# Kernel optimization log

Measured on AMD Instinct MI355X. Metric: run time of the kernel, lower is better.

Reference implementation:

```python
import jax, jax.numpy as jnp
import numpy as np
from math import sqrt

B, L, S, H, E, D = 2, 2048, 2048, 16, 64, 64

def setup_inputs() -> dict:
    key = jax.random.key(0)
    kq, kk, kv = jax.random.split(key, 3)
    queries = jax.random.normal(kq, (B, L, H, E), dtype=jnp.float32)
    keys = jax.random.normal(kk, (B, S, H, E), dtype=jnp.float32)
    values = jax.random.normal(kv, (B, S, H, D), dtype=jnp.float32)
    # causal mask: True where attention is NOT allowed (j > i), matching masked_fill_ semantics
    causal = jnp.triu(jnp.ones((L, S), dtype=jnp.bool_), k=1)
    attn_mask = jnp.broadcast_to(causal[None, None, :, :], (B, 1, L, S))
    return {"queries": queries, "keys": keys, "values": values, "attn_mask": attn_mask}

def reference(queries, keys, values, attn_mask):
    # scores: [B,H,L,S]
    scale = 1.0 / sqrt(queries.shape[-1])
    scores = jnp.einsum('blhe,bshe->bhls', queries, keys)
    scores = jnp.where(attn_mask, -jnp.inf, scores)
    A = jax.nn.softmax(scale * scores, axis=-1)
    V = jnp.einsum('bhls,bshd->blhd', A, values)
    return V
```

## Files before the change

kernel.cpp:

```cpp
#include <hip/hip_runtime.h>

typedef unsigned short ushort_t;
typedef __attribute__((ext_vector_type(8))) short s8v;
typedef __attribute__((ext_vector_type(2))) unsigned u2v;
typedef __attribute__((ext_vector_type(4))) float f4;

__device__ __forceinline__ ushort_t f2bf(float x) {
    unsigned u = __builtin_bit_cast(unsigned, x);
    return (ushort_t)((u + 0x7FFFu + ((u >> 16) & 1u)) >> 16);
}
__device__ __forceinline__ unsigned pack_hi16(float lo, float hi) {
    unsigned a = __builtin_bit_cast(unsigned, lo);
    unsigned b = __builtin_bit_cast(unsigned, hi);
    return (a >> 16) | (b & 0xFFFF0000u);
}

__global__ __launch_bounds__(256) void prep_kv(const float* __restrict__ K,
                                               const float* __restrict__ V,
                                               ushort_t* __restrict__ Kb,
                                               ushort_t* __restrict__ VT) {
    __shared__ ushort_t T[64 * 72];
    if (blockIdx.x < 2048) {
        const int gid = blockIdx.x * 256 + threadIdx.x;
        const int e = (gid & 7) * 8;
        const int h = (gid >> 3) & 15;
        const int s = (gid >> 7) & 2047;
        const int b = gid >> 18;
        const float* src = K + (((b * 2048 + s) * 16 + h) * 64 + e);
        f4 a = *(const f4*)src;
        f4 c = *(const f4*)(src + 4);
        s8v o;
        #pragma unroll
        for (int j = 0; j < 4; ++j) { o[j] = (short)f2bf(a[j]); o[j + 4] = (short)f2bf(c[j]); }
        *(s8v*)(Kb + (((b * 16 + h) * 2048 + s) * 64 + e)) = o;
    } else {
        const int v = blockIdx.x - 2048;
        const int s0 = (v & 31) * 64;
        const int h  = (v >> 5) & 15;
        const int b  = v >> 9;
        const int t  = threadIdx.x;
        {
            const int srow = t >> 2, dc = (t & 3) * 16;
            const float* src = V + (((b * 2048 + s0 + srow) * 16 + h) * 64 + dc);
            #pragma unroll
            for (int c = 0; c < 4; ++c) {
                f4 vv = *(const f4*)(src + c * 4);
                #pragma unroll
                for (int j = 0; j < 4; ++j) T[(dc + c * 4 + j) * 72 + srow] = f2bf(vv[j]);
            }
        }
        __syncthreads();
        {
            const int d = t >> 2, sq = (t & 3) * 16;
            ushort_t* dst = VT + (((b * 16 + h) * 64 + d) * 2048 + s0 + sq);
            *(s8v*)(dst)     = *(const s8v*)(&T[d * 72 + sq]);
            *(s8v*)(dst + 8) = *(const s8v*)(&T[d * 72 + sq + 8]);
        }
    }
}

__global__ __launch_bounds__(128, 2) void fattn_main(
    const float* __restrict__ Q,
    const ushort_t* __restrict__ Kb,
    const ushort_t* __restrict__ VTb,
    float* __restrict__ O)
{
    constexpr float K1 = 0.18033688011112042f;
    constexpr float SHIFT = 12.0f;
    __shared__ ushort_t KT [64 * 72];
    __shared__ ushort_t VTl[64 * 72];
    __shared__ ushort_t P  [4][16 * 72];

    const int bx = blockIdx.x;
    const int bh = bx & 31;
    const int g  = bx >> 5, c8 = g & 7, j4 = g >> 3;
    const int i  = (j4 == 0) ? c8 : (j4 == 1) ? 31 - c8 : (j4 == 2) ? 15 - c8 : 16 + c8;
    const int b = bh >> 4, h = bh & 15;
    const int qr0 = i * 64;
    const int il  = i;

    const int wave = threadIdx.x >> 6;
    const int lane = threadIdx.x & 63;
    const int l15  = lane & 15;
    const int quad = lane >> 4;

    const ushort_t* kb  = Kb  + bh * (2048 * 64);
    const ushort_t* vtb = VTb + bh * (64 * 2048);
    const float*    qb  = Q + b * (2048 * 1024) + h * 64;
    float*          ob  = O + b * (2048 * 1024) + h * 64;

    const s8v ones = {0x3F80, 0x3F80, 0x3F80, 0x3F80, 0x3F80, 0x3F80, 0x3F80, 0x3F80};
    const f4 zero4 = {0.f, 0.f, 0.f, 0.f};

    const int sr = (wave << 5) + (lane >> 1);
    const int sc = (lane & 1) << 5;

    s8v aq[2][2];
    #pragma unroll
    for (int m = 0; m < 2; ++m) {
        const float* qrow = qb + (qr0 + wave * 32 + m * 16 + l15) * 1024;
        #pragma unroll
        for (int ks = 0; ks < 2; ++ks) {
            f4 x = *(const f4*)(qrow + ks * 32 + quad * 8);
            f4 y = *(const f4*)(qrow + ks * 32 + quad * 8 + 4);
            #pragma unroll
            for (int j = 0; j < 4; ++j) {
                aq[m][ks][j]     = (short)f2bf(x[j]);
                aq[m][ks][j + 4] = (short)f2bf(y[j]);
            }
        }
    }

    f4 oacc[2][4];
    f4 lsum[2] = {zero4, zero4};
    #pragma unroll
    for (int m = 0; m < 2; ++m)
        #pragma unroll
        for (int d = 0; d < 4; ++d) oacc[m][d] = zero4;

    s8v gK[4], gV[4];
    {
        const ushort_t* ksrc = kb + sr * 64 + sc;
        const ushort_t* vsrc = vtb + sr * 2048 + sc;
        #pragma unroll
        for (int c = 0; c < 4; ++c) {
            gK[c] = *(const s8v*)(ksrc + c * 8);
            gV[c] = *(const s8v*)(vsrc + c * 8);
        }
    }

    for (int it = 0; it <= il; ++it) {
        #pragma unroll
        for (int c = 0; c < 4; ++c) {
            *(s8v*)&KT [sr * 72 + sc + c * 8] = gK[c];
            *(s8v*)&VTl[sr * 72 + sc + c * 8] = gV[c];
        }
        __syncthreads();

        s8v gK2[4], gV2[4];
        if (it < il) {
            const ushort_t* ksrc = kb + ((it + 1) * 64 + sr) * 64 + sc;
            const ushort_t* vsrc = vtb + sr * 2048 + (it + 1) * 64 + sc;
            #pragma unroll
            for (int c = 0; c < 4; ++c) {
                gK2[c] = *(const s8v*)(ksrc + c * 8);
                gV2[c] = *(const s8v*)(vsrc + c * 8);
            }
        }

        const int n0 = it * 64;
        const bool diag = (it == il);

        f4 st[2][4];
        #pragma unroll
        for (int t = 0; t < 4; ++t) {
            const s8v bk0 = *(const s8v*)&KT[(t * 16 + l15) * 72 + quad * 8];
            const s8v bk1 = *(const s8v*)&KT[(t * 16 + l15) * 72 + 32 + quad * 8];
            #pragma unroll
            for (int m = 0; m < 2; ++m) {
                f4 a = __builtin_amdgcn_mfma_f32_16x16x32_bf16(bk0, aq[m][0], zero4, 0, 0, 0);
                st[m][t] = __builtin_amdgcn_mfma_f32_16x16x32_bf16(bk1, aq[m][1], a, 0, 0, 0);
            }
        }

        #pragma unroll
        for (int m = 0; m < 2; ++m) {
            ushort_t* Pm = P[wave * 2 + m];
            #pragma unroll
            for (int t = 0; t < 4; ++t) {
                float p[4];
                #pragma unroll
                for (int r = 0; r < 4; ++r) {
                    float x = __builtin_fmaf(st[m][t][r], K1, -SHIFT);
                    if (diag) {
                        const int gj = n0 + t * 16 + quad * 4 + r;
                        const int gi = qr0 + wave * 32 + m * 16 + l15;
                        if (gj > gi) x = -INFINITY;
                    }
                    p[r] = __builtin_exp2f(x);
                }
                u2v pk;
                pk[0] = pack_hi16(p[0], p[1]);
                pk[1] = pack_hi16(p[2], p[3]);
                *(u2v*)&Pm[l15 * 72 + t * 16 + quad * 4] = pk;
            }
        }

        #pragma unroll
        for (int ks = 0; ks < 2; ++ks) {
            s8v bvv[4];
            #pragma unroll
            for (int dd = 0; dd < 4; ++dd)
                bvv[dd] = *(const s8v*)&VTl[(dd * 16 + l15) * 72 + ks * 32 + quad * 8];
            #pragma unroll
            for (int m = 0; m < 2; ++m) {
                const s8v ap = *(const s8v*)&P[wave * 2 + m][l15 * 72 + ks * 32 + quad * 8];
                lsum[m] = __builtin_amdgcn_mfma_f32_16x16x32_bf16(ap, ones, lsum[m], 0, 0, 0);
                #pragma unroll
                for (int dd = 0; dd < 4; ++dd)
                    oacc[m][dd] = __builtin_amdgcn_mfma_f32_16x16x32_bf16(ap, bvv[dd], oacc[m][dd], 0, 0, 0);
            }
        }

        __syncthreads();

        if (it < il) {
            #pragma unroll
            for (int c = 0; c < 4; ++c) { gK[c] = gK2[c]; gV[c] = gV2[c]; }
        }
    }

    #pragma unroll
    for (int m = 0; m < 2; ++m)
        #pragma unroll
        for (int r = 0; r < 4; ++r) {
            const float inv = 1.0f / lsum[m][r];
            const int row = qr0 + wave * 32 + m * 16 + quad * 4 + r;
            #pragma unroll
            for (int dd = 0; dd < 4; ++dd)
                ob[row * 1024 + dd * 16 + l15] = oacc[m][dd][r] * inv;
        }
}

#define PSTR 72
__global__ __launch_bounds__(256) void fattn_fallback(
    const float* __restrict__ Q, const float* __restrict__ K,
    const float* __restrict__ V, float* __restrict__ O)
{
    constexpr int strL = 1024, strB = 2048 * strL;
    const float scale = 0.125f;
    __shared__ ushort_t KT[64 * PSTR];
    __shared__ ushort_t VT[64 * PSTR];
    __shared__ ushort_t P[4][16 * PSTR];
    const int bh = blockIdx.x & 31;
    const int b = bh >> 4, h = bh & 15;
    const int im = 31 - (blockIdx.x >> 5);
    const int q0 = im * 64;
    const int tid = threadIdx.x, wave = tid >> 6, lane = tid & 63;
    const int l15 = lane & 15, quad = lane >> 4;
    const float* qbase = Q + b*strB + (q0 + wave*16 + l15)*strL + h*64;
    s8v aq0, aq1;
    {
        f4 q0v = *(const f4*)(qbase + quad*8);
        f4 q1v = *(const f4*)(qbase + quad*8 + 4);
        f4 q2v = *(const f4*)(qbase + 32 + quad*8);
        f4 q3v = *(const f4*)(qbase + 32 + quad*8 + 4);
        #pragma unroll
        for (int j = 0; j < 4; ++j) {
            aq0[j] = (short)f2bf(q0v[j]); aq0[j+4] = (short)f2bf(q1v[j]);
            aq1[j] = (short)f2bf(q2v[j]); aq1[j+4] = (short)f2bf(q3v[j]);
        }
    }
    const f4 zero4 = {0.f,0.f,0.f,0.f};
    f4 oacc[4]; float m_prev[4], lsum[4];
    #pragma unroll
    for (int d = 0; d < 4; ++d) oacc[d] = zero4;
    #pragma unroll
    for (int r = 0; r < 4; ++r) { m_prev[r] = -INFINITY; lsum[r] = 0.0f; }
    const float* kh = K + b*strB + h*64;
    const float* vh = V + b*strB + h*64;
    for (int it = 0; it <= im; ++it) {
        const int n0 = it * 64;
        __syncthreads();
        {
            const float* krow = kh + (n0 + lane)*strL + wave*16;
            f4 k0 = *(const f4*)(krow); f4 k1 = *(const f4*)(krow+4);
            f4 k2 = *(const f4*)(krow+8); f4 k3 = *(const f4*)(krow+12);
            s8v kb0, kb1;
            #pragma unroll
            for (int j = 0; j < 4; ++j) {
                kb0[j] = (short)f2bf(k0[j]); kb0[j+4] = (short)f2bf(k1[j]);
                kb1[j] = (short)f2bf(k2[j]); kb1[j+4] = (short)f2bf(k3[j]);
            }
            *(s8v*)&KT[lane*PSTR + wave*16] = kb0;
            *(s8v*)&KT[lane*PSTR + wave*16 + 8] = kb1;
            const float* vrow = vh + (n0 + lane)*strL + wave*16;
            f4 v0 = *(const f4*)(vrow); f4 v1 = *(const f4*)(vrow+4);
            f4 v2 = *(const f4*)(vrow+8); f4 v3 = *(const f4*)(vrow+12);
            #pragma unroll
            for (int j = 0; j < 4; ++j) {
                VT[(wave*16 + j)*PSTR + lane] = f2bf(v0[j]);
                VT[(wave*16 + 4 + j)*PSTR + lane] = f2bf(v1[j]);
                VT[(wave*16 + 8 + j)*PSTR + lane] = f2bf(v2[j]);
                VT[(wave*16 + 12 + j)*PSTR + lane] = f2bf(v3[j]);
            }
        }
        __syncthreads();
        f4 sacc[4];
        #pragma unroll
        for (int t = 0; t < 4; ++t) {
            sacc[t] = zero4;
            const s8v bk0 = *(const s8v*)&KT[(t*16 + l15)*PSTR + quad*8];
            const s8v bk1 = *(const s8v*)&KT[(t*16 + l15)*PSTR + 32 + quad*8];
            sacc[t] = __builtin_amdgcn_mfma_f32_16x16x32_bf16(aq0, bk0, sacc[t], 0, 0, 0);
            sacc[t] = __builtin_amdgcn_mfma_f32_16x16x32_bf16(aq1, bk1, sacc[t], 0, 0, 0);
        }
        const bool diag = (it == im);
        float sv[4][4], rmax[4];
        #pragma unroll
        for (int r = 0; r < 4; ++r) rmax[r] = -INFINITY;
        #pragma unroll
        for (int t = 0; t < 4; ++t)
            #pragma unroll
            for (int r = 0; r < 4; ++r) {
                float x = sacc[t][r] * scale;
                if (diag) {
                    const int gi = wave*16 + quad*4 + r;
                    const int gj = t*16 + l15;
                    if (gj > gi) x = -INFINITY;
                }
                sv[t][r] = x; rmax[r] = fmaxf(rmax[r], x);
            }
        #pragma unroll
        for (int off = 8; off >= 1; off >>= 1)
            #pragma unroll
            for (int r = 0; r < 4; ++r)
                rmax[r] = fmaxf(rmax[r], __shfl_xor(rmax[r], off, 64));
        float mnew[4], alpha[4], rsum[4];
        #pragma unroll
        for (int r = 0; r < 4; ++r) {
            mnew[r] = fmaxf(m_prev[r], rmax[r]);
            alpha[r] = __expf(m_prev[r] - mnew[r]);
            m_prev[r] = mnew[r]; rsum[r] = 0.f;
        }
        #pragma unroll
        for (int t = 0; t < 4; ++t)
            #pragma unroll
            for (int r = 0; r < 4; ++r) {
                const float p = __expf(sv[t][r] - mnew[r]);
                rsum[r] += p;
                P[wave][(quad*4 + r)*PSTR + t*16 + l15] = f2bf(p);
            }
        #pragma unroll
        for (int off = 8; off >= 1; off >>= 1)
            #pragma unroll
            for (int r = 0; r < 4; ++r)
                rsum[r] += __shfl_xor(rsum[r], off, 64);
        #pragma unroll
        for (int r = 0; r < 4; ++r) lsum[r] = alpha[r]*lsum[r] + rsum[r];
        #pragma unroll
        for (int d = 0; d < 4; ++d)
            #pragma unroll
            for (int r = 0; r < 4; ++r) oacc[d][r] *= alpha[r];
        #pragma unroll
        for (int ks = 0; ks < 2; ++ks) {
            const s8v ap = *(const s8v*)&P[wave][l15*PSTR + ks*32 + quad*8];
            #pragma unroll
            for (int d = 0; d < 4; ++d) {
                const s8v bvv = *(const s8v*)&VT[(d*16 + l15)*PSTR + ks*32 + quad*8];
                oacc[d] = __builtin_amdgcn_mfma_f32_16x16x32_bf16(ap, bvv, oacc[d], 0, 0, 0);
            }
        }
    }
    float* obase = O + b*strB + h*64;
    #pragma unroll
    for (int r = 0; r < 4; ++r) {
        const float inv = 1.0f / lsum[r];
        const int gi = q0 + wave*16 + quad*4 + r;
        #pragma unroll
        for (int d = 0; d < 4; ++d)
            obase[gi*strL + d*16 + l15] = oacc[d][r] * inv;
    }
}

extern "C" void kernel_launch(void* const* d_in, const int* in_sizes, int n_in,
                              void* d_out, int out_size, void* d_ws, size_t ws_size,
                              hipStream_t stream) {
    const float* Q = (const float*)d_in[0];
    const float* K = (const float*)d_in[1];
    const float* V = (const float*)d_in[2];
    float* O = (float*)d_out;
    const size_t NEED = 2ull * 4194304ull * 2ull;
    if (ws_size >= NEED) {
        ushort_t* Kb = (ushort_t*)d_ws;
        ushort_t* VT = Kb + 4194304;
        prep_kv<<<3072, 256, 0, stream>>>(K, V, Kb, VT);
        fattn_main<<<1024, 128, 0, stream>>>(Q, Kb, VT, O);
    } else {
        fattn_fallback<<<1024, 256, 0, stream>>>(Q, K, V, O);
    }
}
```

Before: 153.7 us.

## Pair causal query tiles per block with four waves of sixteen rows

Each block now processes two complementary query tiles (p and 31-p) sequentially, so every block runs exactly 33 KV iterations, balancing causal work across blocks. Block size doubles to 256 threads with each wave owning 16 query rows instead of 32, and the grid halves to 512 blocks. This removes load imbalance from the triangular workload and the tail effect, at the cost of fewer blocks, half the MFMA work per K/V tile load per wave, and a store/reload of Q mid-loop.

```diff
diff --git a/kernel.cpp b/kernel.cpp
--- a/kernel.cpp
+++ b/kernel.cpp
@@ -59,7 +59,7 @@
     }
 }
 
-__global__ __launch_bounds__(128, 2) void fattn_main(
+__global__ __launch_bounds__(256, 2) void fattn_main(
     const float* __restrict__ Q,
     const ushort_t* __restrict__ Kb,
     const ushort_t* __restrict__ VTb,
@@ -73,11 +73,8 @@
 
     const int bx = blockIdx.x;
     const int bh = bx & 31;
-    const int g  = bx >> 5, c8 = g & 7, j4 = g >> 3;
-    const int i  = (j4 == 0) ? c8 : (j4 == 1) ? 31 - c8 : (j4 == 2) ? 15 - c8 : 16 + c8;
+    const int p  = bx >> 5;
     const int b = bh >> 4, h = bh & 15;
-    const int qr0 = i * 64;
-    const int il  = i;
 
     const int wave = threadIdx.x >> 6;
     const int lane = threadIdx.x & 63;
@@ -92,98 +89,102 @@
     const s8v ones = {0x3F80, 0x3F80, 0x3F80, 0x3F80, 0x3F80, 0x3F80, 0x3F80, 0x3F80};
     const f4 zero4 = {0.f, 0.f, 0.f, 0.f};
 
-    const int sr = (wave << 5) + (lane >> 1);
-    const int sc = (lane & 1) << 5;
-
-    s8v aq[2][2];
-    #pragma unroll
-    for (int m = 0; m < 2; ++m) {
-        const float* qrow = qb + (qr0 + wave * 32 + m * 16 + l15) * 1024;
+    const int sr = threadIdx.x >> 2;
+    const int sc = (threadIdx.x & 3) << 4;
+
+    int qr0 = p * 64;
+
+    s8v aq[2];
+    f4 oacc[4];
+    f4 lsum;
+
+    auto loadQ = [&](int qr) {
+        const float* qrow = qb + (qr + wave * 16 + l15) * 1024;
         #pragma unroll
         for (int ks = 0; ks < 2; ++ks) {
             f4 x = *(const f4*)(qrow + ks * 32 + quad * 8);
             f4 y = *(const f4*)(qrow + ks * 32 + quad * 8 + 4);
             #pragma unroll
             for (int j = 0; j < 4; ++j) {
-                aq[m][ks][j]     = (short)f2bf(x[j]);
-                aq[m][ks][j + 4] = (short)f2bf(y[j]);
-            }
-        }
-    }
-
-    f4 oacc[2][4];
-    f4 lsum[2] = {zero4, zero4};
-    #pragma unroll
-    for (int m = 0; m < 2; ++m)
-        #pragma unroll
-        for (int d = 0; d < 4; ++d) oacc[m][d] = zero4;
-
-    s8v gK[4], gV[4];
+                aq[ks][j]     = (short)f2bf(x[j]);
+                aq[ks][j + 4] = (short)f2bf(y[j]);
+            }
+        }
+    };
+    auto zeroAcc = [&]() {
+        lsum = zero4;
+        #pragma unroll
+        for (int d = 0; d < 4; ++d) oacc[d] = zero4;
+    };
+    auto storeO = [&](int qr) {
+        #pragma unroll
+        for (int r = 0; r < 4; ++r) {
+            const float inv = 1.0f / lsum[r];
+            const int row = qr + wave * 16 + quad * 4 + r;
+            #pragma unroll
+            for (int dd = 0; dd < 4; ++dd)
+                ob[row * 1024 + dd * 16 + l15] = oacc[dd][r] * inv;
+        }
+    };
+
+    loadQ(qr0);
+    zeroAcc();
+
+    s8v gK[2], gV[2];
     {
         const ushort_t* ksrc = kb + sr * 64 + sc;
         const ushort_t* vsrc = vtb + sr * 2048 + sc;
-        #pragma unroll
-        for (int c = 0; c < 4; ++c) {
-            gK[c] = *(const s8v*)(ksrc + c * 8);
-            gV[c] = *(const s8v*)(vsrc + c * 8);
-        }
-    }
-
-    for (int it = 0; it <= il; ++it) {
-        #pragma unroll
-        for (int c = 0; c < 4; ++c) {
-            *(s8v*)&KT [sr * 72 + sc + c * 8] = gK[c];
-            *(s8v*)&VTl[sr * 72 + sc + c * 8] = gV[c];
-        }
-        __syncthreads();
-
-        s8v gK2[4], gV2[4];
-        if (it < il) {
-            const ushort_t* ksrc = kb + ((it + 1) * 64 + sr) * 64 + sc;
-            const ushort_t* vsrc = vtb + sr * 2048 + (it + 1) * 64 + sc;
-            #pragma unroll
-            for (int c = 0; c < 4; ++c) {
-                gK2[c] = *(const s8v*)(ksrc + c * 8);
-                gV2[c] = *(const s8v*)(vsrc + c * 8);
-            }
-        }
-
-        const int n0 = it * 64;
-        const bool diag = (it == il);
-
-        f4 st[2][4];
+        gK[0] = *(const s8v*)(ksrc);     gK[1] = *(const s8v*)(ksrc + 8);
+        gV[0] = *(const s8v*)(vsrc);     gV[1] = *(const s8v*)(vsrc + 8);
+    }
+
+    for (int n = 0; n < 33; ++n) {
+        *(s8v*)&KT [sr * 72 + sc]     = gK[0];
+        *(s8v*)&KT [sr * 72 + sc + 8] = gK[1];
+        *(s8v*)&VTl[sr * 72 + sc]     = gV[0];
+        *(s8v*)&VTl[sr * 72 + sc + 8] = gV[1];
+        __syncthreads();
+
+        s8v gK2[2], gV2[2];
+        if (n < 32) {
+            const int sn = (n + 1 <= p) ? (n + 1) : (n - p);
+            const ushort_t* ksrc = kb + (sn * 64 + sr) * 64 + sc;
+            const ushort_t* vsrc = vtb + sr * 2048 + sn * 64 + sc;
+            gK2[0] = *(const s8v*)(ksrc);    gK2[1] = *(const s8v*)(ksrc + 8);
+            gV2[0] = *(const s8v*)(vsrc);    gV2[1] = *(const s8v*)(vsrc + 8);
+        }
+
+        const int s_cur = (n <= p) ? n : (n - p - 1);
+        const int n0 = s_cur * 64;
+        const bool diag = (n == p) || (n == 32);
+
+        f4 st[4];
         #pragma unroll
         for (int t = 0; t < 4; ++t) {
             const s8v bk0 = *(const s8v*)&KT[(t * 16 + l15) * 72 + quad * 8];
             const s8v bk1 = *(const s8v*)&KT[(t * 16 + l15) * 72 + 32 + quad * 8];
-            #pragma unroll
-            for (int m = 0; m < 2; ++m) {
-                f4 a = __builtin_amdgcn_mfma_f32_16x16x32_bf16(bk0, aq[m][0], zero4, 0, 0, 0);
-                st[m][t] = __builtin_amdgcn_mfma_f32_16x16x32_bf16(bk1, aq[m][1], a, 0, 0, 0);
-            }
-        }
-
-        #pragma unroll
-        for (int m = 0; m < 2; ++m) {
-            ushort_t* Pm = P[wave * 2 + m];
-            #pragma unroll
-            for (int t = 0; t < 4; ++t) {
-                float p[4];
-                #pragma unroll
-                for (int r = 0; r < 4; ++r) {
-                    float x = __builtin_fmaf(st[m][t][r], K1, -SHIFT);
-                    if (diag) {
-                        const int gj = n0 + t * 16 + quad * 4 + r;
-                        const int gi = qr0 + wave * 32 + m * 16 + l15;
-                        if (gj > gi) x = -INFINITY;
-                    }
-                    p[r] = __builtin_exp2f(x);
+            f4 a = __builtin_amdgcn_mfma_f32_16x16x32_bf16(bk0, aq[0], zero4, 0, 0, 0);
+            st[t] = __builtin_amdgcn_mfma_f32_16x16x32_bf16(bk1, aq[1], a, 0, 0, 0);
+        }
+
+        ushort_t* Pm = P[wave];
+        #pragma unroll
+        for (int t = 0; t < 4; ++t) {
+            float pv[4];
+            #pragma unroll
+            for (int r = 0; r < 4; ++r) {
+                float x = __builtin_fmaf(st[t][r], K1, -SHIFT);
+                if (diag) {
+                    const int gj = n0 + t * 16 + quad * 4 + r;
+                    const int gi = qr0 + wave * 16 + l15;
+                    if (gj > gi) x = -INFINITY;
                 }
-                u2v pk;
-                pk[0] = pack_hi16(p[0], p[1]);
-                pk[1] = pack_hi16(p[2], p[3]);
-                *(u2v*)&Pm[l15 * 72 + t * 16 + quad * 4] = pk;
-            }
+                pv[r] = __builtin_exp2f(x);
+            }
+            u2v pk;
+            pk[0] = pack_hi16(pv[0], pv[1]);
+            pk[1] = pack_hi16(pv[2], pv[3]);
+            *(u2v*)&Pm[l15 * 72 + t * 16 + quad * 4] = pk;
         }
 
         #pragma unroll
@@ -192,34 +193,29 @@
             #pragma unroll
             for (int dd = 0; dd < 4; ++dd)
                 bvv[dd] = *(const s8v*)&VTl[(dd * 16 + l15) * 72 + ks * 32 + quad * 8];
-            #pragma unroll
-            for (int m = 0; m < 2; ++m) {
-                const s8v ap = *(const s8v*)&P[wave * 2 + m][l15 * 72 + ks * 32 + quad * 8];
-                lsum[m] = __builtin_amdgcn_mfma_f32_16x16x32_bf16(ap, ones, lsum[m], 0, 0, 0);
-                #pragma unroll
-                for (int dd = 0; dd < 4; ++dd)
-                    oacc[m][dd] = __builtin_amdgcn_mfma_f32_16x16x32_bf16(ap, bvv[dd], oacc[m][dd], 0, 0, 0);
-            }
-        }
-
-        __syncthreads();
-
-        if (it < il) {
-            #pragma unroll
-            for (int c = 0; c < 4; ++c) { gK[c] = gK2[c]; gV[c] = gV2[c]; }
-        }
-    }
-
-    #pragma unroll
-    for (int m = 0; m < 2; ++m)
-        #pragma unroll
-        for (int r = 0; r < 4; ++r) {
-            const float inv = 1.0f / lsum[m][r];
-            const int row = qr0 + wave * 32 + m * 16 + quad * 4 + r;
+            const s8v ap = *(const s8v*)&Pm[l15 * 72 + ks * 32 + quad * 8];
+            lsum = __builtin_amdgcn_mfma_f32_16x16x32_bf16(ap, ones, lsum, 0, 0, 0);
             #pragma unroll
             for (int dd = 0; dd < 4; ++dd)
-                ob[row * 1024 + dd * 16 + l15] = oacc[m][dd][r] * inv;
-        }
+                oacc[dd] = __builtin_amdgcn_mfma_f32_16x16x32_bf16(ap, bvv[dd], oacc[dd], 0, 0, 0);
+        }
+
+        __syncthreads();
+
+        if (n < 32) {
+            gK[0] = gK2[0]; gK[1] = gK2[1];
+            gV[0] = gV2[0]; gV[1] = gV2[1];
+        }
+
+        if (n == p) {
+            storeO(qr0);
+            qr0 = (31 - p) * 64;
+            loadQ(qr0);
+            zeroAcc();
+        }
+    }
+
+    storeO(qr0);
 }
 
 #define PSTR 72
@@ -375,7 +371,7 @@
         ushort_t* Kb = (ushort_t*)d_ws;
         ushort_t* VT = Kb + 4194304;
         prep_kv<<<3072, 256, 0, stream>>>(K, V, Kb, VT);
-        fattn_main<<<1024, 128, 0, stream>>>(Q, Kb, VT, O);
+        fattn_main<<<512, 256, 0, stream>>>(Q, Kb, VT, O);
     } else {
         fattn_fallback<<<1024, 256, 0, stream>>>(Q, K, V, O);
     }
```

Result: no change. 151.8 us (-1.2%).

## Pair complementary causal query tiles per block for balanced work

Applied to the files above, without the earlier changes.

Each block now handles query tile p and then tile 31-p in one continuous loop of 33 KV iterations, storing the first tile's output and reloading Q in the middle. The grid halves to 512 blocks, so every block does the same amount of work and the causal triangle no longer leaves uneven tail blocks. In exchange there is less parallelism, 512 blocks of 128 threads on a 256-CU device, and a serial dependency where the Q reload sits inside the loop.

```diff
diff --git a/kernel.cpp b/kernel.cpp
--- a/kernel.cpp
+++ b/kernel.cpp
@@ -73,11 +73,8 @@
 
     const int bx = blockIdx.x;
     const int bh = bx & 31;
-    const int g  = bx >> 5, c8 = g & 7, j4 = g >> 3;
-    const int i  = (j4 == 0) ? c8 : (j4 == 1) ? 31 - c8 : (j4 == 2) ? 15 - c8 : 16 + c8;
+    const int p  = bx >> 5;
     const int b = bh >> 4, h = bh & 15;
-    const int qr0 = i * 64;
-    const int il  = i;
 
     const int wave = threadIdx.x >> 6;
     const int lane = threadIdx.x & 63;
@@ -95,28 +92,51 @@
     const int sr = (wave << 5) + (lane >> 1);
     const int sc = (lane & 1) << 5;
 
+    int qr0 = p * 64;
+
     s8v aq[2][2];
-    #pragma unroll
-    for (int m = 0; m < 2; ++m) {
-        const float* qrow = qb + (qr0 + wave * 32 + m * 16 + l15) * 1024;
-        #pragma unroll
-        for (int ks = 0; ks < 2; ++ks) {
-            f4 x = *(const f4*)(qrow + ks * 32 + quad * 8);
-            f4 y = *(const f4*)(qrow + ks * 32 + quad * 8 + 4);
-            #pragma unroll
-            for (int j = 0; j < 4; ++j) {
-                aq[m][ks][j]     = (short)f2bf(x[j]);
-                aq[m][ks][j + 4] = (short)f2bf(y[j]);
-            }
-        }
-    }
-
     f4 oacc[2][4];
-    f4 lsum[2] = {zero4, zero4};
-    #pragma unroll
-    for (int m = 0; m < 2; ++m)
-        #pragma unroll
-        for (int d = 0; d < 4; ++d) oacc[m][d] = zero4;
+    f4 lsum[2];
+
+    auto loadQ = [&](int qr) {
+        #pragma unroll
+        for (int m = 0; m < 2; ++m) {
+            const float* qrow = qb + (qr + wave * 32 + m * 16 + l15) * 1024;
+            #pragma unroll
+            for (int ks = 0; ks < 2; ++ks) {
+                f4 x = *(const f4*)(qrow + ks * 32 + quad * 8);
+                f4 y = *(const f4*)(qrow + ks * 32 + quad * 8 + 4);
+                #pragma unroll
+                for (int j = 0; j < 4; ++j) {
+                    aq[m][ks][j]     = (short)f2bf(x[j]);
+                    aq[m][ks][j + 4] = (short)f2bf(y[j]);
+                }
+            }
+        }
+    };
+    auto zeroAcc = [&]() {
+        #pragma unroll
+        for (int m = 0; m < 2; ++m) {
+            lsum[m] = zero4;
+            #pragma unroll
+            for (int d = 0; d < 4; ++d) oacc[m][d] = zero4;
+        }
+    };
+    auto storeO = [&](int qr) {
+        #pragma unroll
+        for (int m = 0; m < 2; ++m)
+            #pragma unroll
+            for (int r = 0; r < 4; ++r) {
+                const float inv = 1.0f / lsum[m][r];
+                const int row = qr + wave * 32 + m * 16 + quad * 4 + r;
+                #pragma unroll
+                for (int dd = 0; dd < 4; ++dd)
+                    ob[row * 1024 + dd * 16 + l15] = oacc[m][dd][r] * inv;
+            }
+    };
+
+    loadQ(qr0);
+    zeroAcc();
 
     s8v gK[4], gV[4];
     {
@@ -129,7 +149,7 @@
         }
     }
 
-    for (int it = 0; it <= il; ++it) {
+    for (int n = 0; n < 33; ++n) {
         #pragma unroll
         for (int c = 0; c < 4; ++c) {
             *(s8v*)&KT [sr * 72 + sc + c * 8] = gK[c];
@@ -138,9 +158,10 @@
         __syncthreads();
 
         s8v gK2[4], gV2[4];
-        if (it < il) {
-            const ushort_t* ksrc = kb + ((it + 1) * 64 + sr) * 64 + sc;
-            const ushort_t* vsrc = vtb + sr * 2048 + (it + 1) * 64 + sc;
+        if (n < 32) {
+            const int sn = (n + 1 <= p) ? (n + 1) : (n - p);
+            const ushort_t* ksrc = kb + (sn * 64 + sr) * 64 + sc;
+            const ushort_t* vsrc = vtb + sr * 2048 + sn * 64 + sc;
             #pragma unroll
             for (int c = 0; c < 4; ++c) {
                 gK2[c] = *(const s8v*)(ksrc + c * 8);
@@ -148,8 +169,9 @@
             }
         }
 
-        const int n0 = it * 64;
-        const bool diag = (it == il);
+        const int s_cur = (n <= p) ? n : (n - p - 1);
+        const int n0 = s_cur * 64;
+        const bool diag = (n == p) || (n == 32);
 
         f4 st[2][4];
         #pragma unroll
@@ -168,7 +190,7 @@
             ushort_t* Pm = P[wave * 2 + m];
             #pragma unroll
             for (int t = 0; t < 4; ++t) {
-                float p[4];
+                float pv[4];
                 #pragma unroll
                 for (int r = 0; r < 4; ++r) {
                     float x = __builtin_fmaf(st[m][t][r], K1, -SHIFT);
@@ -177,11 +199,11 @@
                         const int gi = qr0 + wave * 32 + m * 16 + l15;
                         if (gj > gi) x = -INFINITY;
                     }
-                    p[r] = __builtin_exp2f(x);
+                    pv[r] = __builtin_exp2f(x);
                 }
                 u2v pk;
-                pk[0] = pack_hi16(p[0], p[1]);
-                pk[1] = pack_hi16(p[2], p[3]);
+                pk[0] = pack_hi16(pv[0], pv[1]);
+                pk[1] = pack_hi16(pv[2], pv[3]);
                 *(u2v*)&Pm[l15 * 72 + t * 16 + quad * 4] = pk;
             }
         }
@@ -204,22 +226,20 @@
 
         __syncthreads();
 
-        if (it < il) {
+        if (n < 32) {
             #pragma unroll
             for (int c = 0; c < 4; ++c) { gK[c] = gK2[c]; gV[c] = gV2[c]; }
         }
-    }
-
-    #pragma unroll
-    for (int m = 0; m < 2; ++m)
-        #pragma unroll
-        for (int r = 0; r < 4; ++r) {
-            const float inv = 1.0f / lsum[m][r];
-            const int row = qr0 + wave * 32 + m * 16 + quad * 4 + r;
-            #pragma unroll
-            for (int dd = 0; dd < 4; ++dd)
-                ob[row * 1024 + dd * 16 + l15] = oacc[m][dd][r] * inv;
-        }
+
+        if (n == p) {
+            storeO(qr0);
+            qr0 = (31 - p) * 64;
+            loadQ(qr0);
+            zeroAcc();
+        }
+    }
+
+    storeO(qr0);
 }
 
 #define PSTR 72
@@ -375,7 +395,7 @@
         ushort_t* Kb = (ushort_t*)d_ws;
         ushort_t* VT = Kb + 4194304;
         prep_kv<<<3072, 256, 0, stream>>>(K, V, Kb, VT);
-        fattn_main<<<1024, 128, 0, stream>>>(Q, Kb, VT, O);
+        fattn_main<<<512, 128, 0, stream>>>(Q, Kb, VT, O);
     } else {
         fattn_fallback<<<1024, 256, 0, stream>>>(Q, K, V, O);
     }
```

After: 176.4 us. 14.8% more time.
